# Optimization experiments

Measured on AMD Instinct MI355X. Metric: run time of the kernel, lower is better.

## Reference

```python
import jax, jax.numpy as jnp
import numpy as np

SP_BETA = 1.0       # rendering_options.sp_beta
INF_DELTA = 1e10    # use_inf_depth=True -> last delta is 1e10
EPS = 1e-10


def setup_inputs() -> dict:
    key = jax.random.key(0)
    k1, k2, k3 = jax.random.split(key, 3)
    B, R, S, C = 8, 16384, 64, 3  # batch, rays, samples-per-ray, rgb channels
    colors = jax.random.normal(k1, (B, R, S, C), dtype=jnp.float32)
    densities = jax.random.normal(k2, (B, R, S, 1), dtype=jnp.float32)
    # depths must be sorted (increasing) along the sample dimension
    depths = jnp.sort(
        jax.random.uniform(k3, (B, R, S, 1), dtype=jnp.float32, minval=0.1, maxval=6.0),
        axis=2,
    )
    return {"colors": colors, "densities": densities, "depths": depths}


def reference(colors, densities, depths):
    # deltas between consecutive samples, last delta = 1e10 (infinite far plane)
    deltas = depths[:, :, 1:] - depths[:, :, :-1]                      # [B,R,S-1,1]
    deltas = jnp.concatenate(
        [deltas, jnp.full_like(deltas[:, :, :1], INF_DELTA)], axis=2)  # [B,R,S,1]

    # clamp_mode == 'softplus' with beta=1.0: softplus(x*beta)/beta
    dens = jax.nn.softplus(densities * SP_BETA) / SP_BETA              # [B,R,S,1]

    alphas = 1.0 - jnp.exp(-deltas * dens)                             # [B,R,S,1]

    # transmittance: cumulative product of (1-alpha), with leading ones
    trans = jnp.cumprod(1.0 - alphas + EPS, axis=2)                    # [B,R,S,1]
    trans = jnp.concatenate([jnp.ones_like(trans[:, :, :1]), trans], axis=2)  # [B,R,S+1,1]

    final_transmittance = trans[:, :, -1, 0]                           # [B,R]
    weights = alphas * trans[:, :, :-1]                                # [B,R,S,1]

    rgb_final = (weights * colors).sum(axis=2)                         # [B,R,C]
    depth = (weights * depths).sum(axis=2)                             # [B,R,1]
    return rgb_final, depth, weights, final_transmittance
```

## Files before the change

kernel.cpp:

```cpp
#include <hip/hip_runtime.h>

#define INF_DELTA 1e10f
#define RM_EPS 1e-10f
#define LOG2E 1.4426950408889634f

__global__ __launch_bounds__(256) void raymarch_kernel(
    const float* __restrict__ colors,
    const float* __restrict__ densities,
    const float* __restrict__ depths,
    float* __restrict__ rgb_out,
    float* __restrict__ depth_out,
    float* __restrict__ weights_out,
    float* __restrict__ trans_out,
    int n_rays)
{
    const int lane = threadIdx.x & 63;
    const int ray  = blockIdx.x * 4 + (threadIdx.x >> 6);
    if (ray >= n_rays) return;

    const long base = (long)ray * 64 + lane;

    const float d = depths[base];
    const float x = densities[base];
    const float* cptr = colors + (long)ray * 192 + lane * 3;
    const float c0 = cptr[0], c1 = cptr[1], c2 = cptr[2];

    const float d_next = __shfl_down(d, 1, 64);
    const float delta = (lane == 63) ? INF_DELTA : (d_next - d);

    const float q   = __builtin_amdgcn_exp2f(-__builtin_fabsf(x) * LOG2E);
    const float l2  = __builtin_amdgcn_logf(1.0f + q);
    const float sp2 = __builtin_fmaf(__builtin_fmaxf(x, 0.0f), LOG2E, l2);
    const float y   = __builtin_amdgcn_exp2f(-delta * sp2);

    const float alpha = 1.0f - y;
    const float t     = y + RM_EPS;

    float p = t;
    #pragma unroll
    for (int off = 1; off < 64; off <<= 1) {
        const float o = __shfl_up(p, off, 64);
        p *= (lane >= off) ? o : 1.0f;
    }
    float trans_excl = __shfl_up(p, 1, 64);
    if (lane == 0) trans_excl = 1.0f;

    const float w      = alpha * trans_excl;
    const float finalT = __shfl(p, 63, 64);

    weights_out[base] = w;

    float s0 = w * c0, s1 = w * c1, s2 = w * c2, s3 = w * d;
    #pragma unroll
    for (int off = 1; off <= 2; off <<= 1) {
        s0 += __shfl_xor(s0, off, 64);
        s1 += __shfl_xor(s1, off, 64);
        s2 += __shfl_xor(s2, off, 64);
        s3 += __shfl_xor(s3, off, 64);
    }
    const int sel = lane & 3;
    float v = (sel == 0) ? s0 : (sel == 1) ? s1 : (sel == 2) ? s2 : s3;
    #pragma unroll
    for (int off = 4; off < 64; off <<= 1) {
        v += __shfl_xor(v, off, 64);
    }

    if (lane < 3) {
        rgb_out[(long)ray * 3 + lane] = v;
    } else if (lane == 3) {
        depth_out[ray] = v;
    } else if (lane == 4) {
        trans_out[ray] = finalT;
    }
}

extern "C" void kernel_launch(void* const* d_in, const int* in_sizes, int n_in,
                              void* d_out, int out_size, void* d_ws, size_t ws_size,
                              hipStream_t stream) {
    const float* colors    = (const float*)d_in[0];
    const float* densities = (const float*)d_in[1];
    const float* depths    = (const float*)d_in[2];

    const int n_rays = in_sizes[1] / 64;

    float* out      = (float*)d_out;
    float* rgb      = out;
    float* depth_o  = rgb + (long)n_rays * 3;
    float* weights  = depth_o + n_rays;
    float* trans    = weights + (long)n_rays * 64;

    const int blocks = (n_rays + 3) / 4;
    raymarch_kernel<<<blocks, 256, 0, stream>>>(
        colors, densities, depths, rgb, depth_o, weights, trans, n_rays);
}
```

Before: 199.4 us.

## Compute transmittance with a log-space DPP add-scan instead of shuffle multiply-scan

The transmittance cumprod is replaced by an inclusive add-scan of per-sample log2 terms, clamped at log2(eps), built from DPP row shifts and row broadcasts. The exclusive transmittance and the final transmittance come back through exp2. The weighted-sum reductions now use DPP quad permutes, row rotates and a ds_swizzle in place of most __shfl_xor calls. The neighbour depth is loaded directly instead of shuffled, and colours are read as float3. The aim is to cut the ds_bpermute-based cross-lane traffic. The catch is that max(g, log2 eps) only approximates log2(y + eps), so results differ slightly from the reference.

```diff
diff --git a/kernel.cpp b/kernel.cpp
--- a/kernel.cpp
+++ b/kernel.cpp
@@ -1,8 +1,24 @@
 #include <hip/hip_runtime.h>
 
 #define INF_DELTA 1e10f
-#define RM_EPS 1e-10f
 #define LOG2E 1.4426950408889634f
+#define LOG2_EPS -33.219280948873623f
+
+template<int CTRL, int RMASK>
+__device__ __forceinline__ float dpp0(float v) {
+    return __int_as_float(
+        __builtin_amdgcn_update_dpp(0, __float_as_int(v), CTRL, RMASK, 0xF, false));
+}
+
+__device__ __forceinline__ float wave_incl_scan_add(float v) {
+    v += dpp0<0x111, 0xF>(v);
+    v += dpp0<0x112, 0xF>(v);
+    v += dpp0<0x114, 0xF>(v);
+    v += dpp0<0x118, 0xF>(v);
+    v += dpp0<0x142, 0xA>(v);
+    v += dpp0<0x143, 0xC>(v);
+    return v;
+}
 
 __global__ __launch_bounds__(256) void raymarch_kernel(
     const float* __restrict__ colors,
@@ -20,57 +36,51 @@
 
     const long base = (long)ray * 64 + lane;
 
-    const float d = depths[base];
-    const float x = densities[base];
-    const float* cptr = colors + (long)ray * 192 + lane * 3;
-    const float c0 = cptr[0], c1 = cptr[1], c2 = cptr[2];
+    const float d      = depths[base];
+    const float d_next = depths[base + ((lane < 63) ? 1 : 0)];
+    const float x      = densities[base];
+    const float3 c     = *reinterpret_cast<const float3*>(colors + (long)ray * 192 + lane * 3);
 
-    const float d_next = __shfl_down(d, 1, 64);
     const float delta = (lane == 63) ? INF_DELTA : (d_next - d);
 
     const float q   = __builtin_amdgcn_exp2f(-__builtin_fabsf(x) * LOG2E);
     const float l2  = __builtin_amdgcn_logf(1.0f + q);
     const float sp2 = __builtin_fmaf(__builtin_fmaxf(x, 0.0f), LOG2E, l2);
-    const float y   = __builtin_amdgcn_exp2f(-delta * sp2);
+    const float g   = -delta * sp2;
+    const float y   = __builtin_amdgcn_exp2f(g);
+    const float alpha = 1.0f - y;
 
-    const float alpha = 1.0f - y;
-    const float t     = y + RM_EPS;
+    const float llane = __builtin_fmaxf(g, LOG2_EPS);
 
-    float p = t;
-    #pragma unroll
-    for (int off = 1; off < 64; off <<= 1) {
-        const float o = __shfl_up(p, off, 64);
-        p *= (lane >= off) ? o : 1.0f;
-    }
-    float trans_excl = __shfl_up(p, 1, 64);
-    if (lane == 0) trans_excl = 1.0f;
+    const float S          = wave_incl_scan_add(llane);
+    const float trans_excl = __builtin_amdgcn_exp2f(S - llane);
 
-    const float w      = alpha * trans_excl;
-    const float finalT = __shfl(p, 63, 64);
-
+    const float w = alpha * trans_excl;
     weights_out[base] = w;
 
-    float s0 = w * c0, s1 = w * c1, s2 = w * c2, s3 = w * d;
-    #pragma unroll
-    for (int off = 1; off <= 2; off <<= 1) {
-        s0 += __shfl_xor(s0, off, 64);
-        s1 += __shfl_xor(s1, off, 64);
-        s2 += __shfl_xor(s2, off, 64);
-        s3 += __shfl_xor(s3, off, 64);
-    }
+    float s0 = w * c.x, s1 = w * c.y, s2 = w * c.z, s3 = w * d;
+    s0 += dpp0<0xB1, 0xF>(s0);
+    s1 += dpp0<0xB1, 0xF>(s1);
+    s2 += dpp0<0xB1, 0xF>(s2);
+    s3 += dpp0<0xB1, 0xF>(s3);
+    s0 += dpp0<0x4E, 0xF>(s0);
+    s1 += dpp0<0x4E, 0xF>(s1);
+    s2 += dpp0<0x4E, 0xF>(s2);
+    s3 += dpp0<0x4E, 0xF>(s3);
+
     const int sel = lane & 3;
     float v = (sel == 0) ? s0 : (sel == 1) ? s1 : (sel == 2) ? s2 : s3;
-    #pragma unroll
-    for (int off = 4; off < 64; off <<= 1) {
-        v += __shfl_xor(v, off, 64);
-    }
+    v += dpp0<0x124, 0xF>(v);
+    v += dpp0<0x128, 0xF>(v);
+    v += __int_as_float(__builtin_amdgcn_ds_swizzle(__float_as_int(v), 0x401F));
+    v += __shfl_xor(v, 32, 64);
 
     if (lane < 3) {
         rgb_out[(long)ray * 3 + lane] = v;
     } else if (lane == 3) {
         depth_out[ray] = v;
-    } else if (lane == 4) {
-        trans_out[ray] = finalT;
+    } else if (lane == 63) {
+        trans_out[ray] = __builtin_amdgcn_exp2f(S);
     }
 }
 
```

Measured after the change: 198.8 us. About the same (-0.3%).
